# Performance work log

Measured on AMD Instinct MI355X. Metric: run time of the kernel, lower is better.

## Reference

```python
import jax, jax.numpy as jnp
import numpy as np

N = 50000      # nodes
E = 800000     # edges (before self-loops)
IN = 128       # in_channels
HID = 64       # hidden_channels
HEADS = 2
OUT = 64       # out_channels (final layer, heads=1, concat=False)
NEG_SLOPE = 0.2
SM_EPS = 1e-16
BN_EPS = 1e-5


def _gat_layer(h, src, dst, W, a_src, a_dst, b, heads, outc, concat):
    """PyG GATConv (eval mode, self-loops already in src/dst)."""
    n = h.shape[0]
    g = (h @ W).reshape(n, heads, outc)                 # [N,H,C]
    al_s = jnp.sum(g * a_src, axis=-1)                  # [N,H]
    al_d = jnp.sum(g * a_dst, axis=-1)                  # [N,H]
    e = al_s[src] + al_d[dst]                           # [E,H]
    e = jnp.where(e > 0, e, NEG_SLOPE * e)              # LeakyReLU
    m = jax.ops.segment_max(e, dst, num_segments=n)     # segment softmax (stable)
    ee = jnp.exp(e - m[dst])
    s = jax.ops.segment_sum(ee, dst, num_segments=n)
    alpha = ee / (s[dst] + SM_EPS)                      # [E,H]
    out = jax.ops.segment_sum(g[src] * alpha[:, :, None], dst, num_segments=n)  # [N,H,C]
    out = out.reshape(n, heads * outc) if concat else out.mean(axis=1)
    return out + b


def _bn_eval(x, gamma, beta, mean, var):
    return (x - mean) * jax.lax.rsqrt(var + BN_EPS) * gamma + beta


def setup_inputs() -> dict:
    key = jax.random.key(0)
    ks = jax.random.split(key, 32)
    d = {}
    d["x"] = jax.random.normal(ks[0], (N, IN), jnp.float32)
    d["edge_index"] = jax.random.randint(ks[1], (2, E), 0, N, dtype=jnp.int32)
    # layer 0: IN -> HID x HEADS (concat)
    d["W0"] = jax.random.normal(ks[2], (IN, HEADS * HID), jnp.float32) * 0.05
    d["a_src0"] = jax.random.normal(ks[3], (HEADS, HID), jnp.float32) * 0.05
    d["a_dst0"] = jax.random.normal(ks[4], (HEADS, HID), jnp.float32) * 0.05
    d["b0"] = jnp.zeros((HEADS * HID,), jnp.float32)
    d["g0"] = jax.random.uniform(ks[5], (HEADS * HID,), jnp.float32, 0.5, 1.5)
    d["beta0"] = jax.random.normal(ks[6], (HEADS * HID,), jnp.float32) * 0.1
    d["m0"] = jax.random.normal(ks[7], (HEADS * HID,), jnp.float32) * 0.1
    d["v0"] = jax.random.uniform(ks[8], (HEADS * HID,), jnp.float32, 0.5, 1.5)
    # layer 1: HID*HEADS -> HID x HEADS (concat)
    d["W1"] = jax.random.normal(ks[9], (HEADS * HID, HEADS * HID), jnp.float32) * 0.05
    d["a_src1"] = jax.random.normal(ks[10], (HEADS, HID), jnp.float32) * 0.05
    d["a_dst1"] = jax.random.normal(ks[11], (HEADS, HID), jnp.float32) * 0.05
    d["b1"] = jnp.zeros((HEADS * HID,), jnp.float32)
    d["g1"] = jax.random.uniform(ks[12], (HEADS * HID,), jnp.float32, 0.5, 1.5)
    d["beta1"] = jax.random.normal(ks[13], (HEADS * HID,), jnp.float32) * 0.1
    d["m1"] = jax.random.normal(ks[14], (HEADS * HID,), jnp.float32) * 0.1
    d["v1"] = jax.random.uniform(ks[15], (HEADS * HID,), jnp.float32, 0.5, 1.5)
    # layer 2: HID*HEADS -> OUT, heads=1, concat=False
    d["W2"] = jax.random.normal(ks[16], (HEADS * HID, OUT), jnp.float32) * 0.05
    d["a_src2"] = jax.random.normal(ks[17], (1, OUT), jnp.float32) * 0.05
    d["a_dst2"] = jax.random.normal(ks[18], (1, OUT), jnp.float32) * 0.05
    d["b2"] = jnp.zeros((OUT,), jnp.float32)
    return d


def reference(x, edge_index, W0, a_src0, a_dst0, b0, g0, beta0, m0, v0,
              W1, a_src1, a_dst1, b1, g1, beta1, m1, v1,
              W2, a_src2, a_dst2, b2):
    n = x.shape[0]
    loops = jnp.arange(n, dtype=edge_index.dtype)
    src = jnp.concatenate([edge_index[0], loops])   # PyG add_self_loops=True
    dst = jnp.concatenate([edge_index[1], loops])
    h = _gat_layer(x, src, dst, W0, a_src0, a_dst0, b0, HEADS, HID, True)
    h = jax.nn.relu(_bn_eval(h, g0, beta0, m0, v0))   # eval: dropout inactive
    h = _gat_layer(h, src, dst, W1, a_src1, a_dst1, b1, HEADS, HID, True)
    h = jax.nn.relu(_bn_eval(h, g1, beta1, m1, v1))
    out = _gat_layer(h, src, dst, W2, a_src2, a_dst2, b2, 1, OUT, False)
    return out
```

## Files before the change

### kernel.cpp

```cpp
#include <hip/hip_runtime.h>
#include <hip/hip_fp16.h>
#include <cstdint>

#define NEG_SLOPE 0.2f
#define SM_EPS 1e-16f
#define BN_EPS 1e-5f

struct alignas(8) half4v { __half2 lo, hi; };

template <int INC, int OUTC, int H>
__global__ __launch_bounds__(256) void gemm_k(const float* __restrict__ A,
                                              const float* __restrict__ W,
                                              const float* __restrict__ asrc,
                                              const float* __restrict__ adst,
                                              __half* __restrict__ G,
                                              float* __restrict__ als,
                                              float* __restrict__ ald, int nrows) {
  constexpr int TPR  = OUTC / 4;
  constexpr int RS   = 256 / TPR;
  constexpr int ROWS = RS * 4;
  __shared__ float wl[INC * OUTC];
  __shared__ float hl[ROWS * INC];
  for (int i = threadIdx.x * 4; i < INC * OUTC; i += 1024)
    *(float4*)&wl[i] = *(const float4*)&W[i];
  int r  = threadIdx.x / TPR;
  int c0 = (threadIdx.x % TPR) * 4;
  float4 sv = *(const float4*)&asrc[c0];
  float4 dv = *(const float4*)&adst[c0];
  for (int base = blockIdx.x * ROWS; base < nrows; base += gridDim.x * ROWS) {
    __syncthreads();
    int limit = min(ROWS, nrows - base) * INC;
    for (int i = threadIdx.x * 4; i < limit; i += 1024)
      *(float4*)&hl[i] = *(const float4*)&A[(size_t)base * INC + i];
    __syncthreads();
    float acc[4][4];
#pragma unroll
    for (int q = 0; q < 4; q++)
#pragma unroll
      for (int c = 0; c < 4; c++) acc[q][c] = 0.f;
#pragma unroll 8
    for (int k = 0; k < INC; k++) {
      float4 wv = *(float4*)&wl[k * OUTC + c0];
#pragma unroll
      for (int q = 0; q < 4; q++) {
        float h = hl[(r + q * RS) * INC + k];
        acc[q][0] = fmaf(h, wv.x, acc[q][0]);
        acc[q][1] = fmaf(h, wv.y, acc[q][1]);
        acc[q][2] = fmaf(h, wv.z, acc[q][2]);
        acc[q][3] = fmaf(h, wv.w, acc[q][3]);
      }
    }
    float ps[4], pd[4];
#pragma unroll
    for (int q = 0; q < 4; q++) {
      int rq = base + r + q * RS;
      if (rq < nrows) {
        half4v hv;
        hv.lo = __floats2half2_rn(acc[q][0], acc[q][1]);
        hv.hi = __floats2half2_rn(acc[q][2], acc[q][3]);
        *(half4v*)&G[(size_t)rq * OUTC + c0] = hv;
      }
      ps[q] = acc[q][0] * sv.x + acc[q][1] * sv.y + acc[q][2] * sv.z + acc[q][3] * sv.w;
      pd[q] = acc[q][0] * dv.x + acc[q][1] * dv.y + acc[q][2] * dv.z + acc[q][3] * dv.w;
    }
#pragma unroll
    for (int o = 1; o < 16; o <<= 1) {
#pragma unroll
      for (int q = 0; q < 4; q++) {
        ps[q] += __shfl_xor(ps[q], o);
        pd[q] += __shfl_xor(pd[q], o);
      }
    }
    if ((threadIdx.x & 15) == 0) {
      int head = c0 >> 6;
#pragma unroll
      for (int q = 0; q < 4; q++) {
        int rq = base + r + q * RS;
        if (rq < nrows) {
          als[(size_t)rq * H + head] = ps[q];
          ald[(size_t)rq * H + head] = pd[q];
        }
      }
    }
  }
}

__global__ void deg_k(const int* __restrict__ dst, int E_, int n, int* __restrict__ deg) {
  int ET = E_ + n;
  for (int e = blockIdx.x * blockDim.x + threadIdx.x; e < ET; e += gridDim.x * blockDim.x) {
    int dN = (e < E_) ? dst[e] : (e - E_);
    atomicAdd(&deg[dN], 1);
  }
}

__global__ __launch_bounds__(1024) void scan1_k(const int* __restrict__ deg,
                                                int* __restrict__ incl,
                                                int* __restrict__ bsum, int n) {
  __shared__ int sm[1024];
  int i = blockIdx.x * 1024 + threadIdx.x;
  int v = (i < n) ? deg[i] : 0;
  sm[threadIdx.x] = v;
  __syncthreads();
#pragma unroll
  for (int o = 1; o < 1024; o <<= 1) {
    int t = (threadIdx.x >= o) ? sm[threadIdx.x - o] : 0;
    __syncthreads();
    sm[threadIdx.x] += t;
    __syncthreads();
  }
  if (i < n) incl[i] = sm[threadIdx.x];
  if (threadIdx.x == 1023) bsum[blockIdx.x] = sm[1023];
}

__global__ void scan2_k(int* __restrict__ bsum, int nb) {
  int lane = threadIdx.x;
  int v = (lane < nb) ? bsum[lane] : 0;
#pragma unroll
  for (int o = 1; o < 64; o <<= 1) {
    int t = __shfl_up(v, o);
    if (lane >= o) v += t;
  }
  if (lane < nb) bsum[lane] = v;
}

__global__ void scan3_k(const int* __restrict__ incl, const int* __restrict__ bsum,
                        const int* __restrict__ deg, int* __restrict__ rowptr,
                        int* __restrict__ cursor, int n) {
  int i = blockIdx.x * blockDim.x + threadIdx.x;
  if (i < n) {
    int blk = i >> 10;
    int off = blk ? bsum[blk - 1] : 0;
    int r = incl[i] + off;
    rowptr[i + 1] = r;
    cursor[i] = r - deg[i];
  }
  if (i == 0) rowptr[0] = 0;
}

__global__ void csr_fill_k(const int* __restrict__ src, const int* __restrict__ dst,
                           int E_, int n, int* __restrict__ cursor,
                           uint16_t* __restrict__ csr_src) {
  int ET = E_ + n;
  for (int e = blockIdx.x * blockDim.x + threadIdx.x; e < ET; e += gridDim.x * blockDim.x) {
    int sN = (e < E_) ? src[e] : (e - E_);
    int dN = (e < E_) ? dst[e] : (e - E_);
    int pos = atomicAdd(&cursor[dN], 1);
    __builtin_nontemporal_store((uint16_t)sN, &csr_src[pos]);
  }
}

__global__ __launch_bounds__(256) void gat_agg2_k(
    const int* __restrict__ rowptr, const uint16_t* __restrict__ csr_src,
    const float* __restrict__ als, const float* __restrict__ ald,
    const __half* __restrict__ G, const float* __restrict__ bias,
    const float* __restrict__ gamma, const float* __restrict__ beta,
    const float* __restrict__ mean, const float* __restrict__ var,
    float* __restrict__ out, int n) {
  int lane = threadIdx.x & 63;
  int wid  = (blockIdx.x * blockDim.x + threadIdx.x) >> 6;
  int nw   = (gridDim.x * blockDim.x) >> 6;
  for (int node = wid; node < n; node += nw) {
    int beg = rowptr[node];
    int deg = rowptr[node + 1] - beg;
    float2 adp = *(const float2*)&ald[(size_t)node * 2];
    float aAx = 0.f, aAy = 0.f, aBx = 0.f, aBy = 0.f;
    float aCx = 0.f, aCy = 0.f, aDx = 0.f, aDy = 0.f;
    if (deg <= 64) {
      int sl = 0;
      float p0 = 0.f, p1 = 0.f;
      if (lane < deg) {
        sl = csr_src[beg + lane];
        float2 ap = *(const float2*)&als[(size_t)sl * 2];
        float v0 = ap.x + adp.x, v1 = ap.y + adp.y;
        v0 = v0 > 0.f ? v0 : NEG_SLOPE * v0;
        v1 = v1 > 0.f ? v1 : NEG_SLOPE * v1;
        p0 = __expf(v0); p1 = __expf(v1);
      }
      float s0 = p0, s1 = p1;
#pragma unroll
      for (int o = 1; o < 64; o <<= 1) {
        s0 += __shfl_xor(s0, o);
        s1 += __shfl_xor(s1, o);
      }
      float a0 = p0 / (s0 + SM_EPS);
      float a1 = p1 / (s1 + SM_EPS);
      bool hi = (lane >= 32);
      int i = 0;
      for (; i + 4 <= deg; i += 4) {
        int sA = __shfl(sl, i), sB = __shfl(sl, i + 1);
        int sC = __shfl(sl, i + 2), sD = __shfl(sl, i + 3);
        float wA0 = __shfl(a0, i),     wA1 = __shfl(a1, i);
        float wB0 = __shfl(a0, i + 1), wB1 = __shfl(a1, i + 1);
        float wC0 = __shfl(a0, i + 2), wC1 = __shfl(a1, i + 2);
        float wD0 = __shfl(a0, i + 3), wD1 = __shfl(a1, i + 3);
        float wA = hi ? wA1 : wA0, wB = hi ? wB1 : wB0;
        float wC = hi ? wC1 : wC0, wD = hi ? wD1 : wD0;
        float2 gA = __half22float2(*(const __half2*)&G[(size_t)sA * 128 + 2 * lane]);
        float2 gB = __half22float2(*(const __half2*)&G[(size_t)sB * 128 + 2 * lane]);
        float2 gC = __half22float2(*(const __half2*)&G[(size_t)sC * 128 + 2 * lane]);
        float2 gD = __half22float2(*(const __half2*)&G[(size_t)sD * 128 + 2 * lane]);
        aAx = fmaf(wA, gA.x, aAx); aAy = fmaf(wA, gA.y, aAy);
        aBx = fmaf(wB, gB.x, aBx); aBy = fmaf(wB, gB.y, aBy);
        aCx = fmaf(wC, gC.x, aCx); aCy = fmaf(wC, gC.y, aCy);
        aDx = fmaf(wD, gD.x, aDx); aDy = fmaf(wD, gD.y, aDy);
      }
      for (; i < deg; ++i) {
        int   s  = __shfl(sl, i);
        float w0 = __shfl(a0, i), w1 = __shfl(a1, i);
        float w  = hi ? w1 : w0;
        float2 g2 = __half22float2(*(const __half2*)&G[(size_t)s * 128 + 2 * lane]);
        aAx = fmaf(w, g2.x, aAx); aAy = fmaf(w, g2.y, aAy);
      }
    } else {
      float s0 = 0.f, s1 = 0.f;
      for (int i = lane; i < deg; i += 64) {
        int s = csr_src[beg + i];
        float2 ap = *(const float2*)&als[(size_t)s * 2];
        float v0 = ap.x + adp.x; v0 = v0 > 0.f ? v0 : NEG_SLOPE * v0;
        float v1 = ap.y + adp.y; v1 = v1 > 0.f ? v1 : NEG_SLOPE * v1;
        s0 += __expf(v0); s1 += __expf(v1);
      }
#pragma unroll
      for (int o = 1; o < 64; o <<= 1) {
        s0 += __shfl_xor(s0, o);
        s1 += __shfl_xor(s1, o);
      }
      float inv0 = 1.f / (s0 + SM_EPS);
      float inv1 = 1.f / (s1 + SM_EPS);
      bool hi = (lane >= 32);
      for (int i = 0; i < deg; ++i) {
        int s = csr_src[beg + i];
        float2 ap = *(const float2*)&als[(size_t)s * 2];
        float v0 = ap.x + adp.x; v0 = v0 > 0.f ? v0 : NEG_SLOPE * v0;
        float v1 = ap.y + adp.y; v1 = v1 > 0.f ? v1 : NEG_SLOPE * v1;
        float w = hi ? (__expf(v1) * inv1) : (__expf(v0) * inv0);
        float2 g2 = __half22float2(*(const __half2*)&G[(size_t)s * 128 + 2 * lane]);
        aAx = fmaf(w, g2.x, aAx); aAy = fmaf(w, g2.y, aAy);
      }
    }
    float accx = (aAx + aBx) + (aCx + aDx);
    float accy = (aAy + aBy) + (aCy + aDy);
    int j0 = 2 * lane;
    float2 bv = *(const float2*)&bias[j0];
    float2 mv = *(const float2*)&mean[j0];
    float2 vv = *(const float2*)&var[j0];
    float2 gv = *(const float2*)&gamma[j0];
    float2 tv = *(const float2*)&beta[j0];
    float u0 = (accx + bv.x - mv.x) * rsqrtf(vv.x + BN_EPS) * gv.x + tv.x;
    float u1 = (accy + bv.y - mv.y) * rsqrtf(vv.y + BN_EPS) * gv.y + tv.y;
    *(float2*)&out[(size_t)node * 128 + j0] = make_float2(fmaxf(u0, 0.f), fmaxf(u1, 0.f));
  }
}

__global__ __launch_bounds__(256) void gat_agg1_k(
    const int* __restrict__ rowptr, const uint16_t* __restrict__ csr_src,
    const float* __restrict__ als, const float* __restrict__ ald,
    const __half* __restrict__ G, const float* __restrict__ bias,
    float* __restrict__ out, int n) {
  int lane = threadIdx.x & 63;
  int wid  = (blockIdx.x * blockDim.x + threadIdx.x) >> 6;
  int nw   = (gridDim.x * blockDim.x) >> 6;
  for (int node = wid; node < n; node += nw) {
    int beg = rowptr[node];
    int deg = rowptr[node + 1] - beg;
    float ad0 = ald[node];
    float aA = 0.f, aB = 0.f, aC = 0.f, aD = 0.f;
    if (deg <= 64) {
      int sl = 0;
      float p0 = 0.f;
      if (lane < deg) {
        sl = csr_src[beg + lane];
        float v0 = als[sl] + ad0;
        v0 = v0 > 0.f ? v0 : NEG_SLOPE * v0;
        p0 = __expf(v0);
      }
      float s0 = p0;
#pragma unroll
      for (int o = 1; o < 64; o <<= 1) s0 += __shfl_xor(s0, o);
      float a0 = p0 / (s0 + SM_EPS);
      int i = 0;
      for (; i + 4 <= deg; i += 4) {
        int sA = __shfl(sl, i), sB = __shfl(sl, i + 1);
        int sC = __shfl(sl, i + 2), sD = __shfl(sl, i + 3);
        float wA = __shfl(a0, i),     wB = __shfl(a0, i + 1);
        float wC = __shfl(a0, i + 2), wD = __shfl(a0, i + 3);
        float gA = __half2float(G[(size_t)sA * 64 + lane]);
        float gB = __half2float(G[(size_t)sB * 64 + lane]);
        float gC = __half2float(G[(size_t)sC * 64 + lane]);
        float gD = __half2float(G[(size_t)sD * 64 + lane]);
        aA = fmaf(wA, gA, aA); aB = fmaf(wB, gB, aB);
        aC = fmaf(wC, gC, aC); aD = fmaf(wD, gD, aD);
      }
      for (; i < deg; ++i) {
        int   s = __shfl(sl, i);
        float w = __shfl(a0, i);
        aA = fmaf(w, __half2float(G[(size_t)s * 64 + lane]), aA);
      }
    } else {
      float s0 = 0.f;
      for (int i = lane; i < deg; i += 64) {
        int s = csr_src[beg + i];
        float v0 = als[s] + ad0; v0 = v0 > 0.f ? v0 : NEG_SLOPE * v0;
        s0 += __expf(v0);
      }
#pragma unroll
      for (int o = 1; o < 64; o <<= 1) s0 += __shfl_xor(s0, o);
      float inv0 = 1.f / (s0 + SM_EPS);
      for (int i = 0; i < deg; ++i) {
        int s = csr_src[beg + i];
        float v0 = als[s] + ad0; v0 = v0 > 0.f ? v0 : NEG_SLOPE * v0;
        float w = __expf(v0) * inv0;
        aA = fmaf(w, __half2float(G[(size_t)s * 64 + lane]), aA);
      }
    }
    out[(size_t)node * 64 + lane] = ((aA + aB) + (aC + aD)) + bias[lane];
  }
}

extern "C" void kernel_launch(void* const* d_in, const int* in_sizes, int n_in,
                              void* d_out, int out_size, void* d_ws, size_t ws_size,
                              hipStream_t stream) {
  const float* x   = (const float*)d_in[0];
  const int*   ei  = (const int*)d_in[1];
  const float* W0  = (const float*)d_in[2];
  const float* as0 = (const float*)d_in[3];
  const float* ad0 = (const float*)d_in[4];
  const float* b0  = (const float*)d_in[5];
  const float* gm0 = (const float*)d_in[6];
  const float* bt0 = (const float*)d_in[7];
  const float* mu0 = (const float*)d_in[8];
  const float* vr0 = (const float*)d_in[9];
  const float* W1  = (const float*)d_in[10];
  const float* as1 = (const float*)d_in[11];
  const float* ad1 = (const float*)d_in[12];
  const float* b1  = (const float*)d_in[13];
  const float* gm1 = (const float*)d_in[14];
  const float* bt1 = (const float*)d_in[15];
  const float* mu1 = (const float*)d_in[16];
  const float* vr1 = (const float*)d_in[17];
  const float* W2  = (const float*)d_in[18];
  const float* as2 = (const float*)d_in[19];
  const float* ad2 = (const float*)d_in[20];
  const float* b2  = (const float*)d_in[21];

  int N  = in_sizes[0] / 128;
  int E  = in_sizes[1] / 2;
  int ET = E + N;
  const int* srcp = ei;
  const int* dstp = ei + E;

  char* w = (char*)d_ws;
  auto carve = [&](size_t bytes) {
    void* p = (void*)w;
    w += (bytes + 255) & ~(size_t)255;
    return p;
  };
  __half*   G      = (__half*)carve((size_t)N * 128 * 2);
  float*    Hb     = (float*)carve((size_t)N * 128 * 4);
  float*    ALS    = (float*)carve((size_t)N * 2 * 4);
  float*    ALD    = (float*)carve((size_t)N * 2 * 4);
  int*      DEG    = (int*)carve((size_t)N * 4);
  int*      INCL   = (int*)carve((size_t)N * 4);
  int*      BSUM   = (int*)carve((size_t)64 * 4);
  int*      ROWPTR = (int*)carve((size_t)(N + 1) * 4);
  int*      CURSOR = (int*)carve((size_t)N * 4);
  uint16_t* CSRSRC = (uint16_t*)carve((size_t)ET * 2);

  int egrid = min((ET + 255) / 256, 2048);
  int agrid = (N + 3) / 4;
  int nblk  = (N + 1023) / 1024;

  hipMemsetAsync(DEG, 0, (size_t)N * 4, stream);
  deg_k<<<egrid, 256, 0, stream>>>(dstp, E, N, DEG);
  scan1_k<<<nblk, 1024, 0, stream>>>(DEG, INCL, BSUM, N);
  scan2_k<<<1, 64, 0, stream>>>(BSUM, nblk);
  scan3_k<<<(N + 255) / 256, 256, 0, stream>>>(INCL, BSUM, DEG, ROWPTR, CURSOR, N);
  csr_fill_k<<<egrid, 256, 0, stream>>>(srcp, dstp, E, N, CURSOR, CSRSRC);

  gemm_k<128, 128, 2><<<512, 256, 0, stream>>>(x, W0, as0, ad0, G, ALS, ALD, N);
  gat_agg2_k<<<agrid, 256, 0, stream>>>(ROWPTR, CSRSRC, ALS, ALD, G, b0, gm0, bt0,
                                        mu0, vr0, Hb, N);
  gemm_k<128, 128, 2><<<512, 256, 0, stream>>>(Hb, W1, as1, ad1, G, ALS, ALD, N);
  gat_agg2_k<<<agrid, 256, 0, stream>>>(ROWPTR, CSRSRC, ALS, ALD, G, b1, gm1, bt1,
                                        mu1, vr1, Hb, N);
  gemm_k<128, 64, 1><<<512, 256, 0, stream>>>(Hb, W2, as2, ad2, G, ALS, ALD, N);
  gat_agg1_k<<<agrid, 256, 0, stream>>>(ROWPTR, CSRSRC, ALS, ALD, G, b2,
                                        (float*)d_out, N);
}
```

Before: 319.5 us.

## Build sorted CSR per node range and aggregate with half-wave per node

CSR construction is reworked so each block owns a range of destination nodes. It scans the full edge list, fills its rows with LDS cursors instead of global atomics, and then insertion-sorts each row by source id for more regular gathers. The GAT aggregation kernels move from one 64-lane wave per node to 32-lane groups, each lane loading 4 or 2 features at once, which doubles nodes per wave and widens the loads. The cost is that every one of the 256 blocks re-reads the whole edge list, which adds large redundant L2 traffic to CSR build. Nodes with degree between 33 and 64 also fall to the slower two-pass path.

```diff
diff --git a/kernel.cpp b/kernel.cpp
--- a/kernel.cpp
+++ b/kernel.cpp
@@ -124,28 +124,45 @@
 }
 
 __global__ void scan3_k(const int* __restrict__ incl, const int* __restrict__ bsum,
-                        const int* __restrict__ deg, int* __restrict__ rowptr,
-                        int* __restrict__ cursor, int n) {
+                        int* __restrict__ rowptr, int n) {
   int i = blockIdx.x * blockDim.x + threadIdx.x;
   if (i < n) {
     int blk = i >> 10;
     int off = blk ? bsum[blk - 1] : 0;
-    int r = incl[i] + off;
-    rowptr[i + 1] = r;
-    cursor[i] = r - deg[i];
+    rowptr[i + 1] = incl[i] + off;
   }
   if (i == 0) rowptr[0] = 0;
 }
 
-__global__ void csr_fill_k(const int* __restrict__ src, const int* __restrict__ dst,
-                           int E_, int n, int* __restrict__ cursor,
-                           uint16_t* __restrict__ csr_src) {
+__global__ __launch_bounds__(512) void csr_fill_range_k(
+    const int* __restrict__ src, const int* __restrict__ dst, int E_, int n,
+    const int* __restrict__ rowptr, uint16_t* __restrict__ csr_src) {
+  __shared__ int cur[512];
+  int npb = (n + gridDim.x - 1) / gridDim.x;
+  int n0  = blockIdx.x * npb;
+  int n1  = min(n0 + npb, n);
+  if (n0 >= n) return;
+  for (int i = threadIdx.x; i < n1 - n0; i += blockDim.x) cur[i] = rowptr[n0 + i];
+  __syncthreads();
   int ET = E_ + n;
-  for (int e = blockIdx.x * blockDim.x + threadIdx.x; e < ET; e += gridDim.x * blockDim.x) {
-    int sN = (e < E_) ? src[e] : (e - E_);
+  for (int e = threadIdx.x; e < ET; e += blockDim.x) {
     int dN = (e < E_) ? dst[e] : (e - E_);
-    int pos = atomicAdd(&cursor[dN], 1);
-    __builtin_nontemporal_store((uint16_t)sN, &csr_src[pos]);
+    if (dN >= n0 && dN < n1) {
+      int sN = (e < E_) ? src[e] : dN;
+      int pos = atomicAdd(&cur[dN - n0], 1);
+      csr_src[pos] = (uint16_t)sN;
+    }
+  }
+  __syncthreads();
+  for (int t = threadIdx.x; t < n1 - n0; t += blockDim.x) {
+    int beg = rowptr[n0 + t];
+    int end = rowptr[n0 + t + 1];
+    for (int i = beg + 1; i < end; ++i) {
+      uint16_t v = csr_src[i];
+      int j = i - 1;
+      while (j >= beg && csr_src[j] > v) { csr_src[j + 1] = csr_src[j]; --j; }
+      csr_src[j + 1] = v;
+    }
   }
 }
 
@@ -156,20 +173,22 @@
     const float* __restrict__ gamma, const float* __restrict__ beta,
     const float* __restrict__ mean, const float* __restrict__ var,
     float* __restrict__ out, int n) {
-  int lane = threadIdx.x & 63;
-  int wid  = (blockIdx.x * blockDim.x + threadIdx.x) >> 6;
-  int nw   = (gridDim.x * blockDim.x) >> 6;
-  for (int node = wid; node < n; node += nw) {
+  int l   = threadIdx.x & 31;
+  int grp = (blockIdx.x * blockDim.x + threadIdx.x) >> 5;
+  int ng  = (gridDim.x * blockDim.x) >> 5;
+  bool h1 = (l >= 16);
+  int c0  = 4 * l;
+  for (int node = grp; node < n; node += ng) {
     int beg = rowptr[node];
     int deg = rowptr[node + 1] - beg;
     float2 adp = *(const float2*)&ald[(size_t)node * 2];
-    float aAx = 0.f, aAy = 0.f, aBx = 0.f, aBy = 0.f;
-    float aCx = 0.f, aCy = 0.f, aDx = 0.f, aDy = 0.f;
-    if (deg <= 64) {
+    float4 accA = make_float4(0.f, 0.f, 0.f, 0.f);
+    float4 accB = make_float4(0.f, 0.f, 0.f, 0.f);
+    if (deg <= 32) {
       int sl = 0;
       float p0 = 0.f, p1 = 0.f;
-      if (lane < deg) {
-        sl = csr_src[beg + lane];
+      if (l < deg) {
+        sl = csr_src[beg + l];
         float2 ap = *(const float2*)&als[(size_t)sl * 2];
         float v0 = ap.x + adp.x, v1 = ap.y + adp.y;
         v0 = v0 > 0.f ? v0 : NEG_SLOPE * v0;
@@ -178,42 +197,40 @@
       }
       float s0 = p0, s1 = p1;
 #pragma unroll
-      for (int o = 1; o < 64; o <<= 1) {
-        s0 += __shfl_xor(s0, o);
-        s1 += __shfl_xor(s1, o);
+      for (int o = 1; o < 32; o <<= 1) {
+        s0 += __shfl_xor(s0, o, 32);
+        s1 += __shfl_xor(s1, o, 32);
       }
       float a0 = p0 / (s0 + SM_EPS);
       float a1 = p1 / (s1 + SM_EPS);
-      bool hi = (lane >= 32);
       int i = 0;
-      for (; i + 4 <= deg; i += 4) {
-        int sA = __shfl(sl, i), sB = __shfl(sl, i + 1);
-        int sC = __shfl(sl, i + 2), sD = __shfl(sl, i + 3);
-        float wA0 = __shfl(a0, i),     wA1 = __shfl(a1, i);
-        float wB0 = __shfl(a0, i + 1), wB1 = __shfl(a1, i + 1);
-        float wC0 = __shfl(a0, i + 2), wC1 = __shfl(a1, i + 2);
-        float wD0 = __shfl(a0, i + 3), wD1 = __shfl(a1, i + 3);
-        float wA = hi ? wA1 : wA0, wB = hi ? wB1 : wB0;
-        float wC = hi ? wC1 : wC0, wD = hi ? wD1 : wD0;
-        float2 gA = __half22float2(*(const __half2*)&G[(size_t)sA * 128 + 2 * lane]);
-        float2 gB = __half22float2(*(const __half2*)&G[(size_t)sB * 128 + 2 * lane]);
-        float2 gC = __half22float2(*(const __half2*)&G[(size_t)sC * 128 + 2 * lane]);
-        float2 gD = __half22float2(*(const __half2*)&G[(size_t)sD * 128 + 2 * lane]);
-        aAx = fmaf(wA, gA.x, aAx); aAy = fmaf(wA, gA.y, aAy);
-        aBx = fmaf(wB, gB.x, aBx); aBy = fmaf(wB, gB.y, aBy);
-        aCx = fmaf(wC, gC.x, aCx); aCy = fmaf(wC, gC.y, aCy);
-        aDx = fmaf(wD, gD.x, aDx); aDy = fmaf(wD, gD.y, aDy);
+      for (; i + 2 <= deg; i += 2) {
+        int sA = __shfl(sl, i, 32), sB = __shfl(sl, i + 1, 32);
+        float wA0 = __shfl(a0, i, 32),     wA1 = __shfl(a1, i, 32);
+        float wB0 = __shfl(a0, i + 1, 32), wB1 = __shfl(a1, i + 1, 32);
+        float wA = h1 ? wA1 : wA0;
+        float wB = h1 ? wB1 : wB0;
+        half4v gA = *(const half4v*)&G[(size_t)sA * 128 + c0];
+        half4v gB = *(const half4v*)&G[(size_t)sB * 128 + c0];
+        float2 gAl = __half22float2(gA.lo), gAh = __half22float2(gA.hi);
+        float2 gBl = __half22float2(gB.lo), gBh = __half22float2(gB.hi);
+        accA.x = fmaf(wA, gAl.x, accA.x); accA.y = fmaf(wA, gAl.y, accA.y);
+        accA.z = fmaf(wA, gAh.x, accA.z); accA.w = fmaf(wA, gAh.y, accA.w);
+        accB.x = fmaf(wB, gBl.x, accB.x); accB.y = fmaf(wB, gBl.y, accB.y);
+        accB.z = fmaf(wB, gBh.x, accB.z); accB.w = fmaf(wB, gBh.y, accB.w);
       }
       for (; i < deg; ++i) {
-        int   s  = __shfl(sl, i);
-        float w0 = __shfl(a0, i), w1 = __shfl(a1, i);
-        float w  = hi ? w1 : w0;
-        float2 g2 = __half22float2(*(const __half2*)&G[(size_t)s * 128 + 2 * lane]);
-        aAx = fmaf(w, g2.x, aAx); aAy = fmaf(w, g2.y, aAy);
+        int   s  = __shfl(sl, i, 32);
+        float w0 = __shfl(a0, i, 32), w1 = __shfl(a1, i, 32);
+        float w  = h1 ? w1 : w0;
+        half4v gv = *(const half4v*)&G[(size_t)s * 128 + c0];
+        float2 gl = __half22float2(gv.lo), gh = __half22float2(gv.hi);
+        accA.x = fmaf(w, gl.x, accA.x); accA.y = fmaf(w, gl.y, accA.y);
+        accA.z = fmaf(w, gh.x, accA.z); accA.w = fmaf(w, gh.y, accA.w);
       }
     } else {
       float s0 = 0.f, s1 = 0.f;
-      for (int i = lane; i < deg; i += 64) {
+      for (int i = l; i < deg; i += 32) {
         int s = csr_src[beg + i];
         float2 ap = *(const float2*)&als[(size_t)s * 2];
         float v0 = ap.x + adp.x; v0 = v0 > 0.f ? v0 : NEG_SLOPE * v0;
@@ -221,34 +238,37 @@
         s0 += __expf(v0); s1 += __expf(v1);
       }
 #pragma unroll
-      for (int o = 1; o < 64; o <<= 1) {
-        s0 += __shfl_xor(s0, o);
-        s1 += __shfl_xor(s1, o);
+      for (int o = 1; o < 32; o <<= 1) {
+        s0 += __shfl_xor(s0, o, 32);
+        s1 += __shfl_xor(s1, o, 32);
       }
       float inv0 = 1.f / (s0 + SM_EPS);
       float inv1 = 1.f / (s1 + SM_EPS);
-      bool hi = (lane >= 32);
       for (int i = 0; i < deg; ++i) {
         int s = csr_src[beg + i];
         float2 ap = *(const float2*)&als[(size_t)s * 2];
         float v0 = ap.x + adp.x; v0 = v0 > 0.f ? v0 : NEG_SLOPE * v0;
         float v1 = ap.y + adp.y; v1 = v1 > 0.f ? v1 : NEG_SLOPE * v1;
-        float w = hi ? (__expf(v1) * inv1) : (__expf(v0) * inv0);
-        float2 g2 = __half22float2(*(const __half2*)&G[(size_t)s * 128 + 2 * lane]);
-        aAx = fmaf(w, g2.x, aAx); aAy = fmaf(w, g2.y, aAy);
-      }
-    }
-    float accx = (aAx + aBx) + (aCx + aDx);
-    float accy = (aAy + aBy) + (aCy + aDy);
-    int j0 = 2 * lane;
-    float2 bv = *(const float2*)&bias[j0];
-    float2 mv = *(const float2*)&mean[j0];
-    float2 vv = *(const float2*)&var[j0];
-    float2 gv = *(const float2*)&gamma[j0];
-    float2 tv = *(const float2*)&beta[j0];
-    float u0 = (accx + bv.x - mv.x) * rsqrtf(vv.x + BN_EPS) * gv.x + tv.x;
-    float u1 = (accy + bv.y - mv.y) * rsqrtf(vv.y + BN_EPS) * gv.y + tv.y;
-    *(float2*)&out[(size_t)node * 128 + j0] = make_float2(fmaxf(u0, 0.f), fmaxf(u1, 0.f));
+        float w = h1 ? (__expf(v1) * inv1) : (__expf(v0) * inv0);
+        half4v gv = *(const half4v*)&G[(size_t)s * 128 + c0];
+        float2 gl = __half22float2(gv.lo), gh = __half22float2(gv.hi);
+        accA.x = fmaf(w, gl.x, accA.x); accA.y = fmaf(w, gl.y, accA.y);
+        accA.z = fmaf(w, gh.x, accA.z); accA.w = fmaf(w, gh.y, accA.w);
+      }
+    }
+    float4 acc = make_float4(accA.x + accB.x, accA.y + accB.y,
+                             accA.z + accB.z, accA.w + accB.w);
+    float4 bv = *(const float4*)&bias[c0];
+    float4 mv = *(const float4*)&mean[c0];
+    float4 vv = *(const float4*)&var[c0];
+    float4 gv = *(const float4*)&gamma[c0];
+    float4 tv = *(const float4*)&beta[c0];
+    float4 u;
+    u.x = fmaxf((acc.x + bv.x - mv.x) * rsqrtf(vv.x + BN_EPS) * gv.x + tv.x, 0.f);
+    u.y = fmaxf((acc.y + bv.y - mv.y) * rsqrtf(vv.y + BN_EPS) * gv.y + tv.y, 0.f);
+    u.z = fmaxf((acc.z + bv.z - mv.z) * rsqrtf(vv.z + BN_EPS) * gv.z + tv.z, 0.f);
+    u.w = fmaxf((acc.w + bv.w - mv.w) * rsqrtf(vv.w + BN_EPS) * gv.w + tv.w, 0.f);
+    *(float4*)&out[(size_t)node * 128 + c0] = u;
   }
 }
 
@@ -257,63 +277,64 @@
     const float* __restrict__ als, const float* __restrict__ ald,
     const __half* __restrict__ G, const float* __restrict__ bias,
     float* __restrict__ out, int n) {
-  int lane = threadIdx.x & 63;
-  int wid  = (blockIdx.x * blockDim.x + threadIdx.x) >> 6;
-  int nw   = (gridDim.x * blockDim.x) >> 6;
-  for (int node = wid; node < n; node += nw) {
+  int l   = threadIdx.x & 31;
+  int grp = (blockIdx.x * blockDim.x + threadIdx.x) >> 5;
+  int ng  = (gridDim.x * blockDim.x) >> 5;
+  int c0  = 2 * l;
+  for (int node = grp; node < n; node += ng) {
     int beg = rowptr[node];
     int deg = rowptr[node + 1] - beg;
     float ad0 = ald[node];
-    float aA = 0.f, aB = 0.f, aC = 0.f, aD = 0.f;
-    if (deg <= 64) {
+    float2 accA = make_float2(0.f, 0.f), accB = make_float2(0.f, 0.f);
+    if (deg <= 32) {
       int sl = 0;
       float p0 = 0.f;
-      if (lane < deg) {
-        sl = csr_src[beg + lane];
+      if (l < deg) {
+        sl = csr_src[beg + l];
         float v0 = als[sl] + ad0;
         v0 = v0 > 0.f ? v0 : NEG_SLOPE * v0;
         p0 = __expf(v0);
       }
       float s0 = p0;
 #pragma unroll
-      for (int o = 1; o < 64; o <<= 1) s0 += __shfl_xor(s0, o);
+      for (int o = 1; o < 32; o <<= 1) s0 += __shfl_xor(s0, o, 32);
       float a0 = p0 / (s0 + SM_EPS);
       int i = 0;
-      for (; i + 4 <= deg; i += 4) {
-        int sA = __shfl(sl, i), sB = __shfl(sl, i + 1);
-        int sC = __shfl(sl, i + 2), sD = __shfl(sl, i + 3);
-        float wA = __shfl(a0, i),     wB = __shfl(a0, i + 1);
-        float wC = __shfl(a0, i + 2), wD = __shfl(a0, i + 3);
-        float gA = __half2float(G[(size_t)sA * 64 + lane]);
-        float gB = __half2float(G[(size_t)sB * 64 + lane]);
-        float gC = __half2float(G[(size_t)sC * 64 + lane]);
-        float gD = __half2float(G[(size_t)sD * 64 + lane]);
-        aA = fmaf(wA, gA, aA); aB = fmaf(wB, gB, aB);
-        aC = fmaf(wC, gC, aC); aD = fmaf(wD, gD, aD);
+      for (; i + 2 <= deg; i += 2) {
+        int sA = __shfl(sl, i, 32), sB = __shfl(sl, i + 1, 32);
+        float wA = __shfl(a0, i, 32), wB = __shfl(a0, i + 1, 32);
+        float2 gA = __half22float2(*(const __half2*)&G[(size_t)sA * 64 + c0]);
+        float2 gB = __half22float2(*(const __half2*)&G[(size_t)sB * 64 + c0]);
+        accA.x = fmaf(wA, gA.x, accA.x); accA.y = fmaf(wA, gA.y, accA.y);
+        accB.x = fmaf(wB, gB.x, accB.x); accB.y = fmaf(wB, gB.y, accB.y);
       }
       for (; i < deg; ++i) {
-        int   s = __shfl(sl, i);
-        float w = __shfl(a0, i);
-        aA = fmaf(w, __half2float(G[(size_t)s * 64 + lane]), aA);
+        int   s = __shfl(sl, i, 32);
+        float w = __shfl(a0, i, 32);
+        float2 g2 = __half22float2(*(const __half2*)&G[(size_t)s * 64 + c0]);
+        accA.x = fmaf(w, g2.x, accA.x); accA.y = fmaf(w, g2.y, accA.y);
       }
     } else {
       float s0 = 0.f;
-      for (int i = lane; i < deg; i += 64) {
+      for (int i = l; i < deg; i += 32) {
         int s = csr_src[beg + i];
         float v0 = als[s] + ad0; v0 = v0 > 0.f ? v0 : NEG_SLOPE * v0;
         s0 += __expf(v0);
       }
 #pragma unroll
-      for (int o = 1; o < 64; o <<= 1) s0 += __shfl_xor(s0, o);
+      for (int o = 1; o < 32; o <<= 1) s0 += __shfl_xor(s0, o, 32);
       float inv0 = 1.f / (s0 + SM_EPS);
       for (int i = 0; i < deg; ++i) {
         int s = csr_src[beg + i];
         float v0 = als[s] + ad0; v0 = v0 > 0.f ? v0 : NEG_SLOPE * v0;
         float w = __expf(v0) * inv0;
-        aA = fmaf(w, __half2float(G[(size_t)s * 64 + lane]), aA);
-      }
-    }
-    out[(size_t)node * 64 + lane] = ((aA + aB) + (aC + aD)) + bias[lane];
+        float2 g2 = __half22float2(*(const __half2*)&G[(size_t)s * 64 + c0]);
+        accA.x = fmaf(w, g2.x, accA.x); accA.y = fmaf(w, g2.y, accA.y);
+      }
+    }
+    float2 bv = *(const float2*)&bias[c0];
+    *(float2*)&out[(size_t)node * 64 + c0] =
+        make_float2(accA.x + accB.x + bv.x, accA.y + accB.y + bv.y);
   }
 }
 
@@ -363,19 +384,18 @@
   int*      INCL   = (int*)carve((size_t)N * 4);
   int*      BSUM   = (int*)carve((size_t)64 * 4);
   int*      ROWPTR = (int*)carve((size_t)(N + 1) * 4);
-  int*      CURSOR = (int*)carve((size_t)N * 4);
   uint16_t* CSRSRC = (uint16_t*)carve((size_t)ET * 2);
 
   int egrid = min((ET + 255) / 256, 2048);
-  int agrid = (N + 3) / 4;
+  int agrid = (N + 7) / 8;
   int nblk  = (N + 1023) / 1024;
 
   hipMemsetAsync(DEG, 0, (size_t)N * 4, stream);
   deg_k<<<egrid, 256, 0, stream>>>(dstp, E, N, DEG);
   scan1_k<<<nblk, 1024, 0, stream>>>(DEG, INCL, BSUM, N);
   scan2_k<<<1, 64, 0, stream>>>(BSUM, nblk);
-  scan3_k<<<(N + 255) / 256, 256, 0, stream>>>(INCL, BSUM, DEG, ROWPTR, CURSOR, N);
-  csr_fill_k<<<egrid, 256, 0, stream>>>(srcp, dstp, E, N, CURSOR, CSRSRC);
+  scan3_k<<<(N + 255) / 256, 256, 0, stream>>>(INCL, BSUM, ROWPTR, N);
+  csr_fill_range_k<<<256, 512, 0, stream>>>(srcp, dstp, E, N, ROWPTR, CSRSRC);
 
   gemm_k<128, 128, 2><<<512, 256, 0, stream>>>(x, W0, as0, ad0, G, ALS, ALD, N);
   gat_agg2_k<<<agrid, 256, 0, stream>>>(ROWPTR, CSRSRC, ALS, ALD, G, b0, gm0, bt0,
```

Result: slower. 819.6 us (+156.6%).
